# Kernel optimization log

Hardware: AMD Instinct MI355X
Metric: run time of the kernel (lower is better)

Reference implementation:

```python
import jax, jax.numpy as jnp
import numpy as np

B, D, N, M = 64, 128, 400, 50
H, KD = 8, 16
NCONV, K, PAD = 4, 7, 3
MAXTS = 10000.0


def _pe(l):
    # PositionEncoding: freqs/phases interleave sin/cos as sin(pos*f + phase)
    i = np.arange(D)
    freqs = MAXTS ** np.where(i % 2 == 0, -i / D, -(i - 1) / D)
    phases = np.where(i % 2 == 0, 0.0, np.pi / 2)
    pos = np.arange(l)
    return jnp.asarray(np.sin(pos[None, :] * freqs[:, None] + phases[:, None]).astype(np.float32))  # [D, l]


def _ln(x, g, b, eps=1e-6):
    # LayerNorm1d over channel dim of [B, D, L]; torch .std() is unbiased (ddof=1), divides by (std+eps)
    mu = x.mean(axis=1, keepdims=True)
    sd = x.std(axis=1, keepdims=True, ddof=1)
    return g[None, :, None] * (x - mu) / (sd + eps) + b[None, :, None]


def _attn(xT, mask, Wq, bq, Wk, bk, Wv, bv, Wo, bo):
    # xT: [B, L, D]; per-head linears vectorized over the head axis
    q = jnp.einsum('bld,hdk->bhlk', xT, Wq) + bq[None, :, None, :]
    k = jnp.einsum('bld,hdk->bhlk', xT, Wk) + bk[None, :, None, :]
    v = jnp.einsum('bld,hdk->bhlk', xT, Wv) + bv[None, :, None, :]
    sc = jnp.einsum('bhik,bhjk->bhij', q, k) / np.sqrt(KD)
    sc = sc - 1e30 * (1.0 - mask[:, None, None, :])  # mask over key positions
    a = jax.nn.softmax(sc, axis=-1)
    o = jnp.einsum('bhij,bhjk->bhik', a, v)
    o = o.transpose(0, 2, 1, 3).reshape(xT.shape[0], xT.shape[1], H * KD)
    return o @ Wo + bo


def _fwd(context_emb, question_emb, c_mask, q_mask, ln_g, ln_b, dw_w, dw_b, pw_w, pw_b,
         Wq, bq, Wk, bk, Wv, bv, Wo, bo, Wfc, bfc, cq_wc, cq_wq, cq_wm, cq_b):
    def block(x, mask):
        out = x + _pe(x.shape[2])[None]
        for i in range(NCONV):  # fixed small layer loop
            res = out
            h = _ln(out, ln_g, ln_b)
            h = jax.lax.conv_general_dilated(h, dw_w[i], (1,), [(PAD, PAD)],
                                             feature_group_count=D,
                                             dimension_numbers=('NCH', 'OIH', 'NCH')) + dw_b[i][None, :, None]
            h = jnp.einsum('bdl,ed->bel', h, pw_w[i]) + pw_b[i][None, :, None]
            out = jax.nn.relu(h) + res  # eval-mode layer_dropout = inputs + residual
        res = out
        h = _ln(out, ln_g, ln_b)
        h = _attn(h.transpose(0, 2, 1), mask, Wq, bq, Wk, bk, Wv, bv, Wo, bo)
        out = h.transpose(0, 2, 1) + res
        res = out
        h = _ln(out, ln_g, ln_b)
        h = jnp.einsum('bdl,ed->bel', h, Wfc) + bfc[None, :, None]
        return h + res

    C = block(context_emb, c_mask)
    Q = block(question_emb, q_mask)
    C2 = C.transpose(0, 2, 1)  # [B, N, D]
    Q2 = Q.transpose(0, 2, 1)  # [B, M, D]
    # Biaffine similarity W0([Q; C; Q*C]) decomposed (same math, no [B,N*M,3D] materialization)
    S = (C2 @ cq_wc)[:, :, None] + (Q2 @ cq_wq)[:, None, :] \
        + jnp.einsum('bnd,bmd->bnm', C2 * cq_wm, Q2) + cq_b[0]
    S_r = jax.nn.softmax(S - 1e30 * (1.0 - q_mask[:, None, :]), axis=2)
    S_c = jax.nn.softmax(S - 1e30 * (1.0 - c_mask[:, :, None]), axis=1)
    A = S_r @ Q2                                    # context-to-query [B, N, D]
    Bt = jnp.einsum('bnm,bkm->bnk', S_r, S_c) @ C2  # query-to-context (DCN style) [B, N, D]
    return jnp.concatenate([C2, A, C2 * A, C2 * Bt], axis=-1)  # [B, N, 4D]


def setup_inputs() -> dict:
    key = jax.random.key(0)
    ks = jax.random.split(key, 16)
    s = 1.0 / np.sqrt(D)
    return dict(
        context_emb=jax.random.normal(ks[0], (B, D, N), jnp.float32),
        question_emb=jax.random.normal(ks[1], (B, D, M), jnp.float32),
        c_mask=jnp.ones((B, N), jnp.float32),
        q_mask=jnp.ones((B, M), jnp.float32),
        ln_g=jnp.ones((D,), jnp.float32),
        ln_b=jnp.zeros((D,), jnp.float32),
        dw_w=jax.random.normal(ks[2], (NCONV, D, 1, K), jnp.float32) / np.sqrt(K),
        dw_b=jnp.zeros((NCONV, D), jnp.float32),
        pw_w=jax.random.normal(ks[3], (NCONV, D, D), jnp.float32) * s,
        pw_b=jnp.zeros((NCONV, D), jnp.float32),
        Wq=jax.random.normal(ks[4], (H, D, KD), jnp.float32) * s,
        bq=jnp.zeros((H, KD), jnp.float32),
        Wk=jax.random.normal(ks[5], (H, D, KD), jnp.float32) * s,
        bk=jnp.zeros((H, KD), jnp.float32),
        Wv=jax.random.normal(ks[6], (H, D, KD), jnp.float32) * s,
        bv=jnp.zeros((H, KD), jnp.float32),
        Wo=jax.random.normal(ks[7], (H * KD, D), jnp.float32) * s,
        bo=jnp.zeros((D,), jnp.float32),
        Wfc=jax.random.normal(ks[8], (D, D), jnp.float32) * s,
        bfc=jnp.zeros((D,), jnp.float32),
        cq_wc=jax.random.normal(ks[9], (D,), jnp.float32) * s,
        cq_wq=jax.random.normal(ks[10], (D,), jnp.float32) * s,
        cq_wm=jax.random.normal(ks[11], (D,), jnp.float32) * s,
        cq_b=jnp.zeros((1,), jnp.float32),
    )


def reference(context_emb, question_emb, c_mask, q_mask, ln_g, ln_b, dw_w, dw_b, pw_w, pw_b,
              Wq, bq, Wk, bk, Wv, bv, Wo, bo, Wfc, bfc, cq_wc, cq_wq, cq_wm, cq_b):
    return _fwd(context_emb, question_emb, c_mask, q_mask, ln_g, ln_b, dw_w, dw_b, pw_w, pw_b,
                Wq, bq, Wk, bk, Wv, bv, Wo, bo, Wfc, bfc, cq_wc, cq_wq, cq_wm, cq_b)
```

## Files before the change

kernel.cpp:

```cpp
#include <hip/hip_runtime.h>
#include <math.h>

#define BB 64
#define DD 128
#define NN 400
#define MM 50
#define HH 8
#define KDIM 16
#define NC 4
#define KW 7

#define SZ_C (BB * DD * NN)
#define SZ_Q (BB * DD * MM)
#define SSTAT (BB * NN + BB * MM)

__global__ void k_transposeW(const float* __restrict__ pw_w, const float* __restrict__ Wo,
                             const float* __restrict__ Wfc, const float* __restrict__ Wq,
                             const float* __restrict__ Wk, const float* __restrict__ Wv,
                             float* __restrict__ Wcan) {
  int idx = blockIdx.x * 256 + threadIdx.x;
  if (idx >= 9 * 16384) return;
  int m = idx >> 14;
  int r = idx & 16383;
  int d = r >> 7, e = r & 127;
  float v;
  if (m < 4) v = pw_w[m * 16384 + e * 128 + d];
  else if (m == 4) v = Wo[d * 128 + e];
  else if (m == 5) v = Wfc[e * 128 + d];
  else {
    const float* W = (m == 6) ? Wq : (m == 7) ? Wk : Wv;
    v = W[((e >> 4) * 128 + d) * 16 + (e & 15)];
  }
  Wcan[idx] = v;
}

__global__ void k_pestats(const float* __restrict__ xC, const float* __restrict__ xQ,
                          float* __restrict__ yC, float* __restrict__ yQ,
                          float* __restrict__ mu, float* __restrict__ inv) {
  int blk = blockIdx.x;
  const float* x; float* y; int L, l0, b, soff;
  if (blk < 448) { b = blk / 7; l0 = (blk % 7) * 64; x = xC; y = yC; L = NN; soff = 0; }
  else { b = blk - 448; l0 = 0; x = xQ; y = yQ; L = MM; soff = BB * NN; }
  int tid = threadIdx.x;
  int ll = tid & 63;
  int dq = tid >> 6;
  int l = l0 + ll;
  __shared__ float s_sum[4][64], s_sq[4][64];
  float sum = 0.f, sq = 0.f;
  if (l < L) {
    const float* px = x + (size_t)b * DD * L + l;
    float* py = y + (size_t)b * DD * L + l;
    for (int d = dq * 32; d < dq * 32 + 32; ++d) {
      int de = d & ~1;
      float freq = __expf((float)de * (-9.210340371976184f / 128.0f));
      float ph = (d & 1) ? 1.5707963267948966f : 0.0f;
      float v = px[(size_t)d * L] + sinf((float)l * freq + ph);
      py[(size_t)d * L] = v;
      sum += v; sq += v * v;
    }
  }
  s_sum[dq][ll] = sum; s_sq[dq][ll] = sq;
  __syncthreads();
  if (dq == 0 && l < L) {
    float ts = s_sum[0][ll] + s_sum[1][ll] + s_sum[2][ll] + s_sum[3][ll];
    float tq = s_sq[0][ll] + s_sq[1][ll] + s_sq[2][ll] + s_sq[3][ll];
    float m = ts * (1.0f / 128.0f);
    float var = (tq - 128.0f * m * m) * (1.0f / 127.0f);
    float sd = sqrtf(fmaxf(var, 0.f));
    mu[soff + b * L + l] = m;
    inv[soff + b * L + l] = 1.0f / (sd + 1e-6f);
  }
}

__global__ __launch_bounds__(256, 2) void k_convgemm(
    const float* __restrict__ xC, const float* __restrict__ xQ,
    float* __restrict__ outC, float* __restrict__ outQ,
    const float* __restrict__ Wc, const float* __restrict__ pwb,
    const float* __restrict__ dww, const float* __restrict__ dwb,
    const float* __restrict__ muI, const float* __restrict__ invI,
    float* __restrict__ muO, float* __restrict__ invO,
    const float* __restrict__ g, const float* __restrict__ beta) {
  int blk = blockIdx.x;
  int b = blk >> 3, tile = blk & 7;
  const float* x; float* out; int L, l0, soff;
  if (tile < 7) { x = xC; out = outC; L = NN; l0 = tile * 64; soff = 0; }
  else { x = xQ; out = outQ; L = MM; l0 = 0; soff = BB * NN; }
  __shared__ float Wl[32 * 128];
  __shared__ float Xl[32 * 64];
  __shared__ float Sm[70], Si[70];
  int tid = threadIdx.x;
  const float* xb = x + (size_t)b * DD * L;
  for (int t = tid; t < 70; t += 256) {
    int gl = l0 + t - 3;
    bool ok = (gl >= 0 && gl < L);
    Sm[t] = ok ? muI[soff + b * L + gl] : 0.f;
    Si[t] = ok ? invI[soff + b * L + gl] : 0.f;
  }
  float acc[8][4];
  #pragma unroll
  for (int i = 0; i < 8; ++i)
    #pragma unroll
    for (int j = 0; j < 4; ++j) acc[i][j] = 0.f;
  __syncthreads();
  for (int kc = 0; kc < 4; ++kc) {
    int d0 = kc * 32;
    #pragma unroll
    for (int i = 0; i < 4; ++i) {
      int idx = i * 256 + tid;
      ((float4*)Wl)[idx] = ((const float4*)Wc)[(size_t)d0 * 32 + idx];
    }
    #pragma unroll
    for (int r = 0; r < 2; ++r) {
      int k = r * 16 + (tid >> 4);
      int d = d0 + k;
      int c0 = (tid & 15) * 4;
      const float* xrow = xb + (size_t)d * L;
      float gd = g[d], bd = beta[d];
      float wv[7];
      #pragma unroll
      for (int u = 0; u < 7; ++u) wv[u] = dww[d * 7 + u];
      float dbv = dwb[d];
      float xw[10];
      int gbase = l0 + c0 - 3;
      if (gbase >= 1 && gbase + 11 <= L && (((unsigned)(d * L + gbase - 1)) & 3u) == 0u) {
        const float4* p = (const float4*)&xrow[gbase - 1];
        float4 A = p[0], Bv = p[1], Cv = p[2];
        float xr[12] = {A.x, A.y, A.z, A.w, Bv.x, Bv.y, Bv.z, Bv.w, Cv.x, Cv.y, Cv.z, Cv.w};
        #pragma unroll
        for (int s = 0; s < 10; ++s)
          xw[s] = gd * (xr[s + 1] - Sm[c0 + s]) * Si[c0 + s] + bd;
      } else {
        #pragma unroll
        for (int s = 0; s < 10; ++s) {
          int gl = gbase + s;
          float v = 0.f;
          if (gl >= 0 && gl < L)
            v = gd * (xrow[gl] - Sm[c0 + s]) * Si[c0 + s] + bd;
          xw[s] = v;
        }
      }
      float4 o;
      o.x = dbv; o.y = dbv; o.z = dbv; o.w = dbv;
      #pragma unroll
      for (int u = 0; u < 7; ++u) {
        o.x += wv[u] * xw[u];
        o.y += wv[u] * xw[u + 1];
        o.z += wv[u] * xw[u + 2];
        o.w += wv[u] * xw[u + 3];
      }
      *(float4*)&Xl[k * 64 + c0] = o;
    }
    __syncthreads();
    int e0 = (tid >> 4) * 8, cq = (tid & 15) * 4;
    for (int k = 0; k < 32; ++k) {
      const float4* wp = (const float4*)&Wl[k * 128 + e0];
      float4 w0 = wp[0], w1 = wp[1];
      float4 xv = *(const float4*)&Xl[k * 64 + cq];
      float we[8] = {w0.x, w0.y, w0.z, w0.w, w1.x, w1.y, w1.z, w1.w};
      float xe[4] = {xv.x, xv.y, xv.z, xv.w};
      #pragma unroll
      for (int i = 0; i < 8; ++i)
        #pragma unroll
        for (int j = 0; j < 4; ++j) acc[i][j] += we[i] * xe[j];
    }
    __syncthreads();
  }
  int e0 = (tid >> 4) * 8, cq = (tid & 15) * 4;
  float ssum[4], ssq[4];
  #pragma unroll
  for (int j = 0; j < 4; ++j) { ssum[j] = 0.f; ssq[j] = 0.f; }
  #pragma unroll
  for (int i = 0; i < 8; ++i) {
    float bi = pwb[e0 + i];
    float* po = out + ((size_t)b * DD + e0 + i) * L;
    const float* pr = xb + (size_t)(e0 + i) * L;
    #pragma unroll
    for (int j = 0; j < 4; ++j) {
      int l = l0 + cq + j;
      if (l < L) {
        float v = fmaxf(acc[i][j] + bi, 0.f) + pr[l];
        po[l] = v;
        ssum[j] += v; ssq[j] += v * v;
      }
    }
  }
  int grp = tid >> 4;
  #pragma unroll
  for (int j = 0; j < 4; ++j) {
    Xl[grp * 64 + cq + j] = ssum[j];
    Wl[grp * 64 + cq + j] = ssq[j];
  }
  __syncthreads();
  if (tid < 64) {
    int l = l0 + tid;
    if (l < L) {
      float ts = 0.f, tq = 0.f;
      #pragma unroll
      for (int gg = 0; gg < 16; ++gg) { ts += Xl[gg * 64 + tid]; tq += Wl[gg * 64 + tid]; }
      float m = ts * (1.0f / 128.0f);
      float var = (tq - 128.0f * m * m) * (1.0f / 127.0f);
      float sd = sqrtf(fmaxf(var, 0.f));
      muO[soff + b * L + l] = m;
      invO[soff + b * L + l] = 1.0f / (sd + 1e-6f);
    }
  }
}

template <int LNF, int ACT, int STATS>
__global__ __launch_bounds__(256) void k_gemm64(
    const float* __restrict__ xC, const float* __restrict__ xQ,
    float* __restrict__ outC, float* __restrict__ outQ,
    const float* __restrict__ Wc, const float* __restrict__ bias,
    const float* __restrict__ mu, const float* __restrict__ inv,
    float* __restrict__ muO, float* __restrict__ invO,
    const float* __restrict__ g, const float* __restrict__ beta) {
  int blk = blockIdx.x;
  int b = blk >> 3, tile = blk & 7;
  const float* x; float* out; int L, l0, soff;
  if (tile < 7) { x = xC; out = outC; L = NN; l0 = tile * 64; soff = 0; }
  else { x = xQ; out = outQ; L = MM; l0 = 0; soff = BB * NN; }
  __shared__ float Wl[32 * 128];
  __shared__ float Xl[32 * 64];
  int tid = threadIdx.x;
  float acc[8][4];
  #pragma unroll
  for (int i = 0; i < 8; ++i)
    #pragma unroll
    for (int j = 0; j < 4; ++j) acc[i][j] = 0.f;
  const float* xb = x + (size_t)b * DD * L;
  const float* pmu = mu + soff + b * L;
  const float* pin = inv + soff + b * L;
  for (int kc = 0; kc < 4; ++kc) {
    int d0 = kc * 32;
    #pragma unroll
    for (int i = 0; i < 4; ++i) {
      int idx = i * 256 + tid;
      ((float4*)Wl)[idx] = ((const float4*)Wc)[(size_t)d0 * 32 + idx];
    }
    #pragma unroll
    for (int t = 0; t < 8; ++t) {
      int idx = t * 256 + tid;
      int k = idx >> 6, l = idx & 63;
      float v = 0.f;
      int gl = l0 + l;
      if (gl < L) {
        v = xb[(size_t)(d0 + k) * L + gl];
        if (LNF) v = g[d0 + k] * (v - pmu[gl]) * pin[gl] + beta[d0 + k];
      }
      Xl[idx] = v;
    }
    __syncthreads();
    int e0 = (tid >> 4) * 8, cq = (tid & 15) * 4;
    for (int k = 0; k < 32; ++k) {
      const float4* wp = (const float4*)&Wl[k * 128 + e0];
      float4 w0 = wp[0], w1 = wp[1];
      float4 xv = *(const float4*)&Xl[k * 64 + cq];
      float we[8] = {w0.x, w0.y, w0.z, w0.w, w1.x, w1.y, w1.z, w1.w};
      float xe[4] = {xv.x, xv.y, xv.z, xv.w};
      #pragma unroll
      for (int i = 0; i < 8; ++i)
        #pragma unroll
        for (int j = 0; j < 4; ++j) acc[i][j] += we[i] * xe[j];
    }
    __syncthreads();
  }
  int e0 = (tid >> 4) * 8, cq = (tid & 15) * 4;
  float ssum[4], ssq[4];
  #pragma unroll
  for (int j = 0; j < 4; ++j) { ssum[j] = 0.f; ssq[j] = 0.f; }
  #pragma unroll
  for (int i = 0; i < 8; ++i) {
    float bi = bias[e0 + i];
    float* po = out + ((size_t)b * DD + e0 + i) * L;
    #pragma unroll
    for (int j = 0; j < 4; ++j) {
      int l = l0 + cq + j;
      if (l < L) {
        float v = acc[i][j] + bi;
        if (ACT != 0) v += po[l];
        po[l] = v;
        if (STATS) { ssum[j] += v; ssq[j] += v * v; }
      }
    }
  }
  if (STATS) {
    int grp = tid >> 4;
    #pragma unroll
    for (int j = 0; j < 4; ++j) {
      Xl[grp * 64 + cq + j] = ssum[j];
      Wl[grp * 64 + cq + j] = ssq[j];
    }
    __syncthreads();
    if (tid < 64) {
      int l = l0 + tid;
      if (l < L) {
        float ts = 0.f, tq = 0.f;
        #pragma unroll
        for (int gg = 0; gg < 16; ++gg) { ts += Xl[gg * 64 + tid]; tq += Wl[gg * 64 + tid]; }
        float m = ts * (1.0f / 128.0f);
        float var = (tq - 128.0f * m * m) * (1.0f / 127.0f);
        float sd = sqrtf(fmaxf(var, 0.f));
        muO[soff + b * L + l] = m;
        invO[soff + b * L + l] = 1.0f / (sd + 1e-6f);
      }
    }
  }
}

__global__ __launch_bounds__(256) void k_gemm_qkv(
    const float* __restrict__ xC, const float* __restrict__ xQ,
    float* __restrict__ o1C, float* __restrict__ o1Q,
    float* __restrict__ o2C, float* __restrict__ o2Q,
    float* __restrict__ o3C, float* __restrict__ o3Q,
    const float* __restrict__ Wcan,
    const float* __restrict__ bq, const float* __restrict__ bk, const float* __restrict__ bv,
    const float* __restrict__ mu, const float* __restrict__ inv,
    const float* __restrict__ g, const float* __restrict__ beta) {
  int blk0 = blockIdx.x;
  int grp = blk0 >> 9;
  int blk = blk0 & 511;
  const float* Wc = Wcan + (size_t)(6 + grp) * 16384;
  const float* bias = (grp == 0) ? bq : (grp == 1) ? bk : bv;
  float* oC = (grp == 0) ? o1C : (grp == 1) ? o2C : o3C;
  float* oQ = (grp == 0) ? o1Q : (grp == 1) ? o2Q : o3Q;
  int b = blk >> 3, tile = blk & 7;
  const float* x; float* out; int L, l0, soff;
  if (tile < 7) { x = xC; out = oC; L = NN; l0 = tile * 64; soff = 0; }
  else { x = xQ; out = oQ; L = MM; l0 = 0; soff = BB * NN; }
  __shared__ float Wl[32 * 128];
  __shared__ float Xl[32 * 64];
  int tid = threadIdx.x;
  float acc[8][4];
  #pragma unroll
  for (int i = 0; i < 8; ++i)
    #pragma unroll
    for (int j = 0; j < 4; ++j) acc[i][j] = 0.f;
  const float* xb = x + (size_t)b * DD * L;
  const float* pmu = mu + soff + b * L;
  const float* pin = inv + soff + b * L;
  for (int kc = 0; kc < 4; ++kc) {
    int d0 = kc * 32;
    #pragma unroll
    for (int i = 0; i < 4; ++i) {
      int idx = i * 256 + tid;
      ((float4*)Wl)[idx] = ((const float4*)Wc)[(size_t)d0 * 32 + idx];
    }
    #pragma unroll
    for (int t = 0; t < 8; ++t) {
      int idx = t * 256 + tid;
      int k = idx >> 6, l = idx & 63;
      float v = 0.f;
      int gl = l0 + l;
      if (gl < L) {
        v = xb[(size_t)(d0 + k) * L + gl];
        v = g[d0 + k] * (v - pmu[gl]) * pin[gl] + beta[d0 + k];
      }
      Xl[idx] = v;
    }
    __syncthreads();
    int e0 = (tid >> 4) * 8, cq = (tid & 15) * 4;
    for (int k = 0; k < 32; ++k) {
      const float4* wp = (const float4*)&Wl[k * 128 + e0];
      float4 w0 = wp[0], w1 = wp[1];
      float4 xv = *(const float4*)&Xl[k * 64 + cq];
      float we[8] = {w0.x, w0.y, w0.z, w0.w, w1.x, w1.y, w1.z, w1.w};
      float xe[4] = {xv.x, xv.y, xv.z, xv.w};
      #pragma unroll
      for (int i = 0; i < 8; ++i)
        #pragma unroll
        for (int j = 0; j < 4; ++j) acc[i][j] += we[i] * xe[j];
    }
    __syncthreads();
  }
  int e0 = (tid >> 4) * 8, cq = (tid & 15) * 4;
  #pragma unroll
  for (int i = 0; i < 8; ++i) {
    float bi = bias[e0 + i];
    float* po = out + ((size_t)b * DD + e0 + i) * L;
    #pragma unroll
    for (int j = 0; j < 4; ++j) {
      int l = l0 + cq + j;
      if (l < L) po[l] = acc[i][j] + bi;
    }
  }
}

__global__ __launch_bounds__(256) void k_attn2(
    const float* __restrict__ qC, const float* __restrict__ kC, const float* __restrict__ vC,
    const float* __restrict__ qQ, const float* __restrict__ kQ, const float* __restrict__ vQ,
    const float* __restrict__ cmask, const float* __restrict__ qmask,
    float* __restrict__ oC, float* __restrict__ oQ) {
  int blk = blockIdx.x;
  const float *qp, *kp, *vp, *mk; float* op; int L, b, h, q0, qcnt;
  if (blk < 1024) {
    b = blk >> 4; h = (blk >> 1) & 7; int half = blk & 1;
    qp = qC; kp = kC; vp = vC; mk = cmask; op = oC; L = NN;
    q0 = half * 256; qcnt = half ? (NN - 256) : 256;
  } else {
    int bb = blk - 1024; b = bb >> 3; h = bb & 7;
    qp = qQ; kp = kQ; vp = vQ; mk = qmask; op = oQ; L = MM;
    q0 = 0; qcnt = MM;
  }
  __shared__ float Kl[NN * KDIM];
  __shared__ float Vl[NN * KDIM];
  __shared__ float Ml[NN];
  int tid = threadIdx.x;
  size_t base = ((size_t)b * DD + h * KDIM) * L;
  int KP = (L + 7) & ~7;
  for (int idx = tid; idx < KDIM * L; idx += 256) {
    int t = idx / L, j = idx - t * L;
    Kl[j * KDIM + t] = kp[base + (size_t)t * L + j];
    Vl[j * KDIM + t] = vp[base + (size_t)t * L + j];
  }
  for (int idx = tid; idx < (KP - L) * KDIM; idx += 256) {
    int j = L + (idx >> 4), t = idx & 15;
    Kl[j * KDIM + t] = 0.f; Vl[j * KDIM + t] = 0.f;
  }
  for (int j = tid; j < KP; j += 256)
    Ml[j] = (j < L) ? -1e30f * (1.0f - mk[b * L + j]) : -1e30f;
  __syncthreads();
  if (tid >= qcnt) return;

  int i = q0 + tid;
  float q[KDIM];
  #pragma unroll
  for (int t = 0; t < KDIM; ++t) q[t] = qp[base + (size_t)t * L + i] * 0.25f;
  float m = -1e30f, ls = 0.f;
  float acc[KDIM];
  #pragma unroll
  for (int t = 0; t < KDIM; ++t) acc[t] = 0.f;
  for (int j0 = 0; j0 < KP; j0 += 8) {
    const float4* mp = (const float4*)&Ml[j0];
    float4 ma0 = mp[0], ma1 = mp[1];
    float mav[8] = {ma0.x, ma0.y, ma0.z, ma0.w, ma1.x, ma1.y, ma1.z, ma1.w};
    float s[8];
    #pragma unroll
    for (int jj = 0; jj < 8; ++jj) {
      const float4* kf = (const float4*)&Kl[(j0 + jj) * KDIM];
      float4 k0 = kf[0], k1 = kf[1], k2 = kf[2], k3 = kf[3];
      float da = q[0] * k0.x + q[1] * k0.y + q[2] * k0.z + q[3] * k0.w
               + q[4] * k1.x + q[5] * k1.y + q[6] * k1.z + q[7] * k1.w;
      float db = q[8] * k2.x + q[9] * k2.y + q[10] * k2.z + q[11] * k2.w
               + q[12] * k3.x + q[13] * k3.y + q[14] * k3.z + q[15] * k3.w;
      s[jj] = da + db + mav[jj];
    }
    float cm = s[0];
    #pragma unroll
    for (int jj = 1; jj < 8; ++jj) cm = fmaxf(cm, s[jj]);
    if (cm > m) {
      float sc = __expf(m - cm);
      ls *= sc;
      #pragma unroll
      for (int t = 0; t < KDIM; ++t) acc[t] *= sc;
      m = cm;
    }
    #pragma unroll
    for (int jj = 0; jj < 8; ++jj) {
      float p = __expf(s[jj] - m);
      ls += p;
      const float4* vf = (const float4*)&Vl[(j0 + jj) * KDIM];
      float4 v0 = vf[0], v1 = vf[1], v2 = vf[2], v3 = vf[3];
      acc[0] += p * v0.x;  acc[1] += p * v0.y;  acc[2] += p * v0.z;  acc[3] += p * v0.w;
      acc[4] += p * v1.x;  acc[5] += p * v1.y;  acc[6] += p * v1.z;  acc[7] += p * v1.w;
      acc[8] += p * v2.x;  acc[9] += p * v2.y;  acc[10] += p * v2.z; acc[11] += p * v2.w;
      acc[12] += p * v3.x; acc[13] += p * v3.y; acc[14] += p * v3.z; acc[15] += p * v3.w;
    }
  }
  float invl = 1.0f / ls;
  #pragma unroll
  for (int t = 0; t < KDIM; ++t)
    op[base + (size_t)t * L + i] = acc[t] * invl;
}

__global__ void k_prep(const float* __restrict__ Cb, const float* __restrict__ Qb,
                       float* __restrict__ C2, float* __restrict__ Q2,
                       const float* __restrict__ wc, const float* __restrict__ wq,
                       float* __restrict__ cd, float* __restrict__ qd) {
  int blk = blockIdx.x, tid = threadIdx.x;
  if (blk < 3840) {
    const float* X; float* Y; int L, rem;
    if (blk < 3328) { X = Cb; Y = C2; L = NN; rem = blk; }
    else { X = Qb; Y = Q2; L = MM; rem = blk - 3328; }
    int ntl = (L + 31) / 32;
    int b = rem / (4 * ntl);
    int r2 = rem % (4 * ntl);
    int d0 = (r2 / ntl) * 32;
    int l0 = (r2 % ntl) * 32;
    __shared__ float T[32][33];
    int c = tid & 31, r8 = tid >> 5;
    const float* xb = X + (size_t)b * DD * L;
    #pragma unroll
    for (int k = 0; k < 4; ++k) {
      int r = r8 + k * 8;
      int l = l0 + c;
      T[r][c] = (l < L) ? xb[(size_t)(d0 + r) * L + l] : 0.f;
    }
    __syncthreads();
    float* yb = Y + (size_t)b * L * DD;
    #pragma unroll
    for (int k = 0; k < 4; ++k) {
      int rr = r8 + k * 8;
      int l = l0 + rr;
      if (l < L) yb[(size_t)l * DD + d0 + c] = T[c][rr];
    }
  } else if (blk < 3940) {
    int idx = (blk - 3840) * 256 + tid;
    if (idx < BB * NN) {
      int l = idx % NN, b = idx / NN;
      const float* px = Cb + (size_t)b * DD * NN + l;
      float acc = 0.f;
      for (int d = 0; d < DD; ++d) acc += px[(size_t)d * NN] * wc[d];
      cd[idx] = acc;
    }
  } else {
    int idx = (blk - 3940) * 256 + tid;
    if (idx < BB * MM) {
      int l = idx % MM, b = idx / MM;
      const float* px = Qb + (size_t)b * DD * MM + l;
      float acc = 0.f;
      for (int d = 0; d < DD; ++d) acc += px[(size_t)d * MM] * wq[d];
      qd[idx] = acc;
    }
  }
}

__global__ __launch_bounds__(256) void k_S2(
    const float* __restrict__ C2, const float* __restrict__ Q2,
    const float* __restrict__ cd, const float* __restrict__ qd,
    const float* __restrict__ wm, const float* __restrict__ bias,
    float* __restrict__ S) {
  int blk = blockIdx.x;
  int b = blk / 7, nt = blk % 7;
  int n0 = nt * 64;
  int nv = NN - n0; if (nv > 64) nv = 64;
  __shared__ float Cw[64 * 132];
  __shared__ float Ql[52 * 132];
  __shared__ float cdl[64];
  __shared__ float qdl[50];
  int tid = threadIdx.x;
  const float4* c4g = (const float4*)(C2 + (size_t)b * NN * DD);
  const float4* q4g = (const float4*)(Q2 + (size_t)b * MM * DD);
  const float4* w4 = (const float4*)wm;
  for (int i = tid; i < 64 * 32; i += 256) {
    int n = i >> 5, d4 = i & 31;
    float4 v = {0.f, 0.f, 0.f, 0.f};
    if (n < nv) {
      float4 c = c4g[(size_t)(n0 + n) * 32 + d4];
      float4 w = w4[d4];
      v.x = c.x * w.x; v.y = c.y * w.y; v.z = c.z * w.z; v.w = c.w * w.w;
    }
    *(float4*)&Cw[n * 132 + d4 * 4] = v;
  }
  for (int i = tid; i < 52 * 32; i += 256) {
    int m = i >> 5, d4 = i & 31;
    float4 v = {0.f, 0.f, 0.f, 0.f};
    if (m < MM) v = q4g[(size_t)m * 32 + d4];
    *(float4*)&Ql[m * 132 + d4 * 4] = v;
  }
  if (tid < 64) cdl[tid] = (tid < nv) ? cd[b * NN + n0 + tid] : 0.f;
  if (tid >= 64 && tid < 114) qdl[tid - 64] = qd[b * MM + (tid - 64)];
  __syncthreads();
  int n = tid >> 2, mg = tid & 3;
  int m0 = mg * 13;
  float acc[13];
  #pragma unroll
  for (int k = 0; k < 13; ++k) acc[k] = 0.f;
  const float* cp = &Cw[n * 132];
  for (int d4 = 0; d4 < 32; ++d4) {
    float4 c = *(const float4*)&cp[d4 * 4];
    #pragma unroll
    for (int k = 0; k < 13; ++k) {
      float4 q = *(const float4*)&Ql[(m0 + k) * 132 + d4 * 4];
      acc[k] += c.x * q.x + c.y * q.y + c.z * q.z + c.w * q.w;
    }
  }
  if (n < nv) {
    float add = cdl[n] + bias[0];
    float* ps = S + ((size_t)b * NN + n0 + n) * MM + m0;
    #pragma unroll
    for (int k = 0; k < 13; ++k) {
      int m = m0 + k;
      if (m < MM) ps[k] = acc[k] + add + qdl[m];
    }
  }
}

__global__ void k_smax(const float* __restrict__ S, float* __restrict__ Sr,
                       float* __restrict__ Sc, const float* __restrict__ cmask,
                       const float* __restrict__ qmask) {
  int blk = blockIdx.x;
  int tid = threadIdx.x;
  if (blk < BB * MM) {
    int b = blk / MM;
    int mcol = blk % MM;
    float vals[7];
    float mx = -1e30f;
    #pragma unroll
    for (int c = 0; c < 7; ++c) {
      int n = tid + c * 64;
      float s = -1e30f;
      if (n < NN)
        s = S[((size_t)b * NN + n) * MM + mcol] - 1e30f * (1.0f - cmask[b * NN + n]);
      vals[c] = s;
      mx = fmaxf(mx, s);
    }
    #pragma unroll
    for (int off = 1; off < 64; off <<= 1) mx = fmaxf(mx, __shfl_xor(mx, off));
    float sum = 0.f;
    #pragma unroll
    for (int c = 0; c < 7; ++c) { vals[c] = __expf(vals[c] - mx); sum += vals[c]; }
    #pragma unroll
    for (int off = 1; off < 64; off <<= 1) sum += __shfl_xor(sum, off);
    float inv = 1.0f / sum;
    #pragma unroll
    for (int c = 0; c < 7; ++c) {
      int n = tid + c * 64;
      if (n < NN) Sc[((size_t)b * NN + n) * MM + mcol] = vals[c] * inv;
    }
  } else {
    int bn = blk - BB * MM;
    int b = bn / NN;
    float s = -1e30f;
    if (tid < MM)
      s = S[(size_t)bn * MM + tid] - 1e30f * (1.0f - qmask[b * MM + tid]);
    float mx = s;
    #pragma unroll
    for (int off = 1; off < 64; off <<= 1) mx = fmaxf(mx, __shfl_xor(mx, off));
    float e = (tid < MM) ? __expf(s - mx) : 0.f;
    float sum = e;
    #pragma unroll
    for (int off = 1; off < 64; off <<= 1) sum += __shfl_xor(sum, off);
    if (tid < MM) Sr[(size_t)bn * MM + tid] = e / sum;
  }
}

__global__ void k_U(const float* __restrict__ Sc, const float* __restrict__ C2,
                    float* __restrict__ U) {
  int idx = blockIdx.x * 256 + threadIdx.x;
  if (idx >= BB * MM * 32) return;
  int d4 = idx & 31;
  int rest = idx >> 5;
  int mcol = rest % MM;
  int b = rest / MM;
  const float* psc = Sc + (size_t)b * NN * MM + mcol;
  const float4* pc2 = (const float4*)(C2 + (size_t)b * NN * DD) + d4;
  float4 acc = {0.f, 0.f, 0.f, 0.f};
  #pragma unroll 4
  for (int kk = 0; kk < NN; ++kk) {
    float s = psc[(size_t)kk * MM];
    float4 c = pc2[(size_t)kk * 32];
    acc.x += s * c.x; acc.y += s * c.y; acc.z += s * c.z; acc.w += s * c.w;
  }
  ((float4*)U)[idx] = acc;
}

__global__ __launch_bounds__(256) void k_ABtF(
    const float* __restrict__ Sr, const float* __restrict__ Q2,
    const float* __restrict__ Uu, const float* __restrict__ C2,
    float* __restrict__ out) {
  int blk = blockIdx.x;
  int b = blk / 7, nt = blk % 7;
  int n0 = nt * 64;
  int nv = NN - n0; if (nv > 64) nv = 64;
  __shared__ float Ql[MM * 128];
  __shared__ float Ul[MM * 128];
  __shared__ float Sl[64 * MM];
  int tid = threadIdx.x;
  const float4* q4 = (const float4*)(Q2 + (size_t)b * MM * DD);
  const float4* u4 = (const float4*)(Uu + (size_t)b * MM * DD);
  for (int i = tid; i < MM * 32; i += 256) {
    ((float4*)Ql)[i] = q4[i];
    ((float4*)Ul)[i] = u4[i];
  }
  for (int i = tid; i < 64 * MM; i += 256) {
    int n = i / MM;
    Sl[i] = (n < nv) ? Sr[((size_t)b * NN + n0 + n) * MM + (i - n * MM)] : 0.f;
  }
  __syncthreads();
  int n = tid >> 2;
  if (n >= nv) return;
  int d04 = (tid & 3) * 8;
  float4 accA[8], accB[8];
  #pragma unroll
  for (int r = 0; r < 8; ++r) {
    accA[r] = {0.f, 0.f, 0.f, 0.f};
    accB[r] = {0.f, 0.f, 0.f, 0.f};
  }
  const float* sp = &Sl[n * MM];
  for (int m = 0; m < MM; ++m) {
    float s = sp[m];
    const float4* qp = (const float4*)&Ql[m * 128] + d04;
    const float4* up = (const float4*)&Ul[m * 128] + d04;
    #pragma unroll
    for (int r = 0; r < 8; ++r) {
      float4 q = qp[r], u = up[r];
      accA[r].x += s * q.x; accA[r].y += s * q.y; accA[r].z += s * q.z; accA[r].w += s * q.w;
      accB[r].x += s * u.x; accB[r].y += s * u.y; accB[r].z += s * u.z; accB[r].w += s * u.w;
    }
  }
  int gn = n0 + n;
  const float4* c4 = (const float4*)(C2 + ((size_t)b * NN + gn) * DD) + d04;
  float4* po = (float4*)(out + (size_t)(b * NN + gn) * 512);
  #pragma unroll
  for (int r = 0; r < 8; ++r) {
    float4 c = c4[r];
    float4 a = accA[r], bt = accB[r];
    po[d04 + r] = c;
    po[32 + d04 + r] = a;
    float4 ca = {c.x * a.x, c.y * a.y, c.z * a.z, c.w * a.w};
    po[64 + d04 + r] = ca;
    float4 cb = {c.x * bt.x, c.y * bt.y, c.z * bt.z, c.w * bt.w};
    po[96 + d04 + r] = cb;
  }
}

extern "C" void kernel_launch(void* const* d_in, const int* in_sizes, int n_in,
                              void* d_out, int out_size, void* d_ws, size_t ws_size,
                              hipStream_t stream) {
  (void)in_sizes; (void)n_in; (void)out_size; (void)ws_size;
  const float* ctx   = (const float*)d_in[0];
  const float* que   = (const float*)d_in[1];
  const float* cmask = (const float*)d_in[2];
  const float* qmask = (const float*)d_in[3];
  const float* ln_g  = (const float*)d_in[4];
  const float* ln_b  = (const float*)d_in[5];
  const float* dw_w  = (const float*)d_in[6];
  const float* dw_b  = (const float*)d_in[7];
  const float* pw_w  = (const float*)d_in[8];
  const float* pw_b  = (const float*)d_in[9];
  const float* Wq    = (const float*)d_in[10];
  const float* bq    = (const float*)d_in[11];
  const float* Wk    = (const float*)d_in[12];
  const float* bk    = (const float*)d_in[13];
  const float* Wv    = (const float*)d_in[14];
  const float* bv    = (const float*)d_in[15];
  const float* Wo    = (const float*)d_in[16];
  const float* bo    = (const float*)d_in[17];
  const float* Wfc   = (const float*)d_in[18];
  const float* bfc   = (const float*)d_in[19];
  const float* cq_wc = (const float*)d_in[20];
  const float* cq_wq = (const float*)d_in[21];
  const float* cq_wm = (const float*)d_in[22];
  const float* cq_b  = (const float*)d_in[23];
  float* out = (float*)d_out;
  float* ws = (float*)d_ws;

  float* Cb   = ws;
  float* Qb   = Cb + SZ_C;
  float* t1C  = Qb + SZ_Q;
  float* t1Q  = t1C + SZ_C;
  float* t2C  = t1Q + SZ_Q;
  float* t2Q  = t2C + SZ_C;
  float* t3C  = t2Q + SZ_Q;
  float* t3Q  = t3C + SZ_C;
  float* t4C  = t3Q + SZ_Q;
  float* t4Q  = t4C + SZ_C;
  float* mu0  = t4Q + SZ_Q;
  float* inv0 = mu0 + SSTAT;
  float* mu1  = inv0 + SSTAT;
  float* inv1 = mu1 + SSTAT;
  float* Wcan = inv1 + SSTAT;

  k_transposeW<<<(9 * 16384 + 255) / 256, 256, 0, stream>>>(pw_w, Wo, Wfc, Wq, Wk, Wv, Wcan);
  k_pestats<<<512, 256, 0, stream>>>(ctx, que, Cb, Qb, mu0, inv0);

  for (int i = 0; i < NC; ++i) {
    const float* inC = (i & 1) ? t1C : Cb;
    const float* inQ = (i & 1) ? t1Q : Qb;
    float* oC = (i & 1) ? Cb : t1C;
    float* oQ = (i & 1) ? Qb : t1Q;
    const float* mI = (i & 1) ? mu1 : mu0;
    const float* iI = (i & 1) ? inv1 : inv0;
    float* mO = (i & 1) ? mu0 : mu1;
    float* iO = (i & 1) ? inv0 : inv1;
    k_convgemm<<<512, 256, 0, stream>>>(inC, inQ, oC, oQ,
                                        Wcan + (size_t)i * 16384, pw_b + (size_t)i * DD,
                                        dw_w + (size_t)i * DD * KW, dw_b + (size_t)i * DD,
                                        mI, iI, mO, iO, ln_g, ln_b);
  }
  k_gemm_qkv<<<1536, 256, 0, stream>>>(Cb, Qb, t1C, t1Q, t2C, t2Q, t3C, t3Q,
                                       Wcan, bq, bk, bv, mu0, inv0, ln_g, ln_b);
  k_attn2<<<1536, 256, 0, stream>>>(t1C, t2C, t3C, t1Q, t2Q, t3Q, cmask, qmask, t4C, t4Q);
  k_gemm64<0, 1, 1><<<512, 256, 0, stream>>>(t4C, t4Q, Cb, Qb, Wcan + 4 * 16384, bo,
                                             mu0, inv0, mu1, inv1, ln_g, ln_b);
  k_gemm64<1, 1, 0><<<512, 256, 0, stream>>>(Cb, Qb, Cb, Qb, Wcan + 5 * 16384, bfc,
                                             mu1, inv1, mu0, inv0, ln_g, ln_b);

  float* C2  = t1C;
  float* Q2  = t1Q;
  float* S   = t2C;
  float* Sr  = t2C + 1638400;
  float* Scb = t3C;
  float* Uu  = t2Q;
  float* cd  = t3Q;
  float* qd  = t4Q;

  k_prep<<<3953, 256, 0, stream>>>(Cb, Qb, C2, Q2, cq_wc, cq_wq, cd, qd);
  k_S2<<<448, 256, 0, stream>>>(C2, Q2, cd, qd, cq_wm, cq_b, S);
  k_smax<<<BB * MM + BB * NN, 64, 0, stream>>>(S, Sr, Scb, cmask, qmask);
  k_U<<<(BB * MM * 32 + 255) / 256, 256, 0, stream>>>(Scb, C2, Uu);
  k_ABtF<<<448, 256, 0, stream>>>(Sr, Q2, Uu, C2, out);
}
```

Baseline: 644.2 us.

## Fuse transpose and dot-products into FC GEMM epilogue; fuse column softmax with U

The final FC GEMM now writes its output tile transposed through shared memory into the C2/Q2 layouts and computes the cq_wc/cq_wq dot products in its epilogue, which removes the separate k_prep kernel and its extra pass over the activations. The column softmax kernel now keeps its normalized column in shared memory and computes U directly, dropping the Sc write/read and the k_U launch. The costs are larger shared-memory tiles in the GEMM, and a U computation done by only 64-thread blocks, each looping serially over 400 rows.

```diff
diff --git a/kernel.cpp b/kernel.cpp
--- a/kernel.cpp
+++ b/kernel.cpp
@@ -206,21 +206,24 @@
   }
 }
 
-template <int LNF, int ACT, int STATS>
+template <int LNF, int ACT, int STATS, int TRANS>
 __global__ __launch_bounds__(256) void k_gemm64(
     const float* __restrict__ xC, const float* __restrict__ xQ,
     float* __restrict__ outC, float* __restrict__ outQ,
     const float* __restrict__ Wc, const float* __restrict__ bias,
     const float* __restrict__ mu, const float* __restrict__ inv,
     float* __restrict__ muO, float* __restrict__ invO,
-    const float* __restrict__ g, const float* __restrict__ beta) {
+    const float* __restrict__ g, const float* __restrict__ beta,
+    float* __restrict__ C2o, float* __restrict__ Q2o,
+    float* __restrict__ cdo, float* __restrict__ qdo,
+    const float* __restrict__ wc, const float* __restrict__ wq) {
   int blk = blockIdx.x;
   int b = blk >> 3, tile = blk & 7;
   const float* x; float* out; int L, l0, soff;
   if (tile < 7) { x = xC; out = outC; L = NN; l0 = tile * 64; soff = 0; }
   else { x = xQ; out = outQ; L = MM; l0 = 0; soff = BB * NN; }
-  __shared__ float Wl[32 * 128];
-  __shared__ float Xl[32 * 64];
+  __shared__ float Wl[TRANS ? 64 * 68 : 32 * 128];
+  __shared__ float Xl[TRANS ? 64 * 68 : 32 * 64];
   int tid = threadIdx.x;
   float acc[8][4];
   #pragma unroll
@@ -280,6 +283,10 @@
         if (ACT != 0) v += po[l];
         po[l] = v;
         if (STATS) { ssum[j] += v; ssq[j] += v * v; }
+        if (TRANS) {
+          float* T = (e0 < 64) ? Wl : Xl;
+          T[(cq + j) * 68 + (e0 & 63) + i] = v;
+        }
       }
     }
   }
@@ -304,6 +311,30 @@
         invO[soff + b * L + l] = 1.0f / (sd + 1e-6f);
       }
     }
+  }
+  if (TRANS) {
+    __syncthreads();
+    int r = tid >> 2, seg = tid & 3;
+    int gl = l0 + r;
+    const float* wsel = (tile < 7) ? wc : wq;
+    float* Y2 = (tile < 7) ? C2o : Q2o;
+    float* dd = (tile < 7) ? cdo : qdo;
+    float part = 0.f;
+    if (gl < L) {
+      float4* dst = (float4*)(Y2 + ((size_t)b * L + gl) * 128);
+      #pragma unroll
+      for (int q8 = 0; q8 < 8; ++q8) {
+        int e = seg * 32 + q8 * 4;
+        const float* T = (e < 64) ? Wl : Xl;
+        float4 v4 = *(const float4*)&T[r * 68 + (e & 63)];
+        dst[seg * 8 + q8] = v4;
+        float4 w4 = *(const float4*)&wsel[e];
+        part += v4.x * w4.x + v4.y * w4.y + v4.z * w4.z + v4.w * w4.w;
+      }
+    }
+    part += __shfl_xor(part, 1);
+    part += __shfl_xor(part, 2);
+    if (gl < L && seg == 0) dd[b * L + gl] = part;
   }
 }
 
@@ -472,58 +503,6 @@
     op[base + (size_t)t * L + i] = acc[t] * invl;
 }
 
-__global__ void k_prep(const float* __restrict__ Cb, const float* __restrict__ Qb,
-                       float* __restrict__ C2, float* __restrict__ Q2,
-                       const float* __restrict__ wc, const float* __restrict__ wq,
-                       float* __restrict__ cd, float* __restrict__ qd) {
-  int blk = blockIdx.x, tid = threadIdx.x;
-  if (blk < 3840) {
-    const float* X; float* Y; int L, rem;
-    if (blk < 3328) { X = Cb; Y = C2; L = NN; rem = blk; }
-    else { X = Qb; Y = Q2; L = MM; rem = blk - 3328; }
-    int ntl = (L + 31) / 32;
-    int b = rem / (4 * ntl);
-    int r2 = rem % (4 * ntl);
-    int d0 = (r2 / ntl) * 32;
-    int l0 = (r2 % ntl) * 32;
-    __shared__ float T[32][33];
-    int c = tid & 31, r8 = tid >> 5;
-    const float* xb = X + (size_t)b * DD * L;
-    #pragma unroll
-    for (int k = 0; k < 4; ++k) {
-      int r = r8 + k * 8;
-      int l = l0 + c;
-      T[r][c] = (l < L) ? xb[(size_t)(d0 + r) * L + l] : 0.f;
-    }
-    __syncthreads();
-    float* yb = Y + (size_t)b * L * DD;
-    #pragma unroll
-    for (int k = 0; k < 4; ++k) {
-      int rr = r8 + k * 8;
-      int l = l0 + rr;
-      if (l < L) yb[(size_t)l * DD + d0 + c] = T[c][rr];
-    }
-  } else if (blk < 3940) {
-    int idx = (blk - 3840) * 256 + tid;
-    if (idx < BB * NN) {
-      int l = idx % NN, b = idx / NN;
-      const float* px = Cb + (size_t)b * DD * NN + l;
-      float acc = 0.f;
-      for (int d = 0; d < DD; ++d) acc += px[(size_t)d * NN] * wc[d];
-      cd[idx] = acc;
-    }
-  } else {
-    int idx = (blk - 3940) * 256 + tid;
-    if (idx < BB * MM) {
-      int l = idx % MM, b = idx / MM;
-      const float* px = Qb + (size_t)b * DD * MM + l;
-      float acc = 0.f;
-      for (int d = 0; d < DD; ++d) acc += px[(size_t)d * MM] * wq[d];
-      qd[idx] = acc;
-    }
-  }
-}
-
 __global__ __launch_bounds__(256) void k_S2(
     const float* __restrict__ C2, const float* __restrict__ Q2,
     const float* __restrict__ cd, const float* __restrict__ qd,
@@ -585,14 +564,15 @@
   }
 }
 
-__global__ void k_smax(const float* __restrict__ S, float* __restrict__ Sr,
-                       float* __restrict__ Sc, const float* __restrict__ cmask,
-                       const float* __restrict__ qmask) {
+__global__ void k_smaxU(const float* __restrict__ S, float* __restrict__ Sr,
+                        const float* __restrict__ cmask, const float* __restrict__ qmask,
+                        const float* __restrict__ C2, float* __restrict__ U) {
   int blk = blockIdx.x;
   int tid = threadIdx.x;
   if (blk < BB * MM) {
     int b = blk / MM;
     int mcol = blk % MM;
+    __shared__ float Sl[NN];
     float vals[7];
     float mx = -1e30f;
     #pragma unroll
@@ -615,8 +595,18 @@
     #pragma unroll
     for (int c = 0; c < 7; ++c) {
       int n = tid + c * 64;
-      if (n < NN) Sc[((size_t)b * NN + n) * MM + mcol] = vals[c] * inv;
-    }
+      if (n < NN) Sl[n] = vals[c] * inv;
+    }
+    __syncthreads();
+    const float2* c2 = (const float2*)(C2 + (size_t)b * NN * DD) + tid;
+    float2 a = {0.f, 0.f};
+    #pragma unroll 4
+    for (int kk = 0; kk < NN; ++kk) {
+      float s = Sl[kk];
+      float2 c = c2[(size_t)kk * 64];
+      a.x += s * c.x; a.y += s * c.y;
+    }
+    ((float2*)(U + ((size_t)b * MM + mcol) * DD))[tid] = a;
   } else {
     int bn = blk - BB * MM;
     int b = bn / NN;
@@ -632,26 +622,6 @@
     for (int off = 1; off < 64; off <<= 1) sum += __shfl_xor(sum, off);
     if (tid < MM) Sr[(size_t)bn * MM + tid] = e / sum;
   }
-}
-
-__global__ void k_U(const float* __restrict__ Sc, const float* __restrict__ C2,
-                    float* __restrict__ U) {
-  int idx = blockIdx.x * 256 + threadIdx.x;
-  if (idx >= BB * MM * 32) return;
-  int d4 = idx & 31;
-  int rest = idx >> 5;
-  int mcol = rest % MM;
-  int b = rest / MM;
-  const float* psc = Sc + (size_t)b * NN * MM + mcol;
-  const float4* pc2 = (const float4*)(C2 + (size_t)b * NN * DD) + d4;
-  float4 acc = {0.f, 0.f, 0.f, 0.f};
-  #pragma unroll 4
-  for (int kk = 0; kk < NN; ++kk) {
-    float s = psc[(size_t)kk * MM];
-    float4 c = pc2[(size_t)kk * 32];
-    acc.x += s * c.x; acc.y += s * c.y; acc.z += s * c.z; acc.w += s * c.w;
-  }
-  ((float4*)U)[idx] = acc;
 }
 
 __global__ __launch_bounds__(256) void k_ABtF(
@@ -781,23 +751,24 @@
   k_gemm_qkv<<<1536, 256, 0, stream>>>(Cb, Qb, t1C, t1Q, t2C, t2Q, t3C, t3Q,
                                        Wcan, bq, bk, bv, mu0, inv0, ln_g, ln_b);
   k_attn2<<<1536, 256, 0, stream>>>(t1C, t2C, t3C, t1Q, t2Q, t3Q, cmask, qmask, t4C, t4Q);
-  k_gemm64<0, 1, 1><<<512, 256, 0, stream>>>(t4C, t4Q, Cb, Qb, Wcan + 4 * 16384, bo,
-                                             mu0, inv0, mu1, inv1, ln_g, ln_b);
-  k_gemm64<1, 1, 0><<<512, 256, 0, stream>>>(Cb, Qb, Cb, Qb, Wcan + 5 * 16384, bfc,
-                                             mu1, inv1, mu0, inv0, ln_g, ln_b);
 
   float* C2  = t1C;
   float* Q2  = t1Q;
   float* S   = t2C;
   float* Sr  = t2C + 1638400;
-  float* Scb = t3C;
   float* Uu  = t2Q;
   float* cd  = t3Q;
-  float* qd  = t4Q;
-
-  k_prep<<<3953, 256, 0, stream>>>(Cb, Qb, C2, Q2, cq_wc, cq_wq, cd, qd);
+  float* qd  = t4Q + SZ_Q - BB * MM;
+
+  k_gemm64<0, 1, 1, 0><<<512, 256, 0, stream>>>(t4C, t4Q, Cb, Qb, Wcan + 4 * 16384, bo,
+                                                mu0, inv0, mu1, inv1, ln_g, ln_b,
+                                                nullptr, nullptr, nullptr, nullptr,
+                                                nullptr, nullptr);
+  k_gemm64<1, 1, 0, 1><<<512, 256, 0, stream>>>(Cb, Qb, Cb, Qb, Wcan + 5 * 16384, bfc,
+                                                mu1, inv1, mu0, inv0, ln_g, ln_b,
+                                                C2, Q2, cd, qd, cq_wc, cq_wq);
+
   k_S2<<<448, 256, 0, stream>>>(C2, Q2, cd, qd, cq_wm, cq_b, S);
-  k_smax<<<BB * MM + BB * NN, 64, 0, stream>>>(S, Sr, Scb, cmask, qmask);
-  k_U<<<(BB * MM * 32 + 255) / 256, 256, 0, stream>>>(Scb, C2, Uu);
+  k_smaxU<<<BB * MM + BB * NN, 64, 0, stream>>>(S, Sr, cmask, qmask, C2, Uu);
   k_ABtF<<<448, 256, 0, stream>>>(Sr, Q2, Uu, C2, out);
 }
```

After: 621.0 us, median of 2. -3.6%, faster.
